# Kernel tuning notes

Measured on AMD Instinct MI355X. Metric: run time of the kernel, lower is better.

The kernel has to match this reference:

```python
import math
import jax
import jax.numpy as jnp
import numpy as np
from jax import lax
from jax.scipy.special import digamma

EPS_RHO = 1e-12
EPS_LOG = 1e-8
BANDWIDTH_FACTOR = 1.06
MIN_BANDWIDTH = 1e-4


def setup_inputs() -> dict:
    key = jax.random.key(0)
    activity = jax.random.uniform(key, (1024, 64), dtype=jnp.float32)  # values in [0,1]
    return {"activity": activity, "k": 5}


def _knn_joint_entropy(activity, k):
    B, N = activity.shape
    # (B, B, N) pairwise differences -> squared distances (B, B)
    diff = activity[:, None, :] - activity[None, :, :]
    dists_sq = jnp.sum(diff * diff, axis=-1)
    # k+1 smallest per row (includes self-distance 0); torch.topk(largest=False) ascending
    neg_topk, _ = lax.top_k(-dists_sq, k + 1)
    rho_sq = jnp.maximum(-neg_topk[:, k], EPS_RHO)
    # log unit-ball volume via lgamma (avoids overflow for large N)
    log_c_d = 0.5 * N * math.log(math.pi) - math.lgamma(N / 2 + 1)
    dg_k = digamma(jnp.float32(k))
    dg_B = digamma(jnp.float32(B))
    log_rho_sum = 0.5 * jnp.mean(jnp.log(rho_sq))
    h_nats = -dg_k + dg_B + log_c_d + N * log_rho_sum
    return h_nats / math.log(2.0)


def _kde_density(samples, query_points, bandwidth_factor):
    B_samples, R = samples.shape
    std = jnp.std(samples, axis=0, ddof=1)  # torch.std uses unbiased (ddof=1)
    h = jnp.maximum(bandwidth_factor * std * B_samples ** (-0.2), MIN_BANDWIDTH)  # (R,)
    X = query_points[:, None, :]  # (B, 1, R)
    Y = samples[None, :, :]       # (1, B, R)
    hr = h[None, None, :]
    norm_factor = math.sqrt(2 * math.pi)
    u_orig = (X - Y) / hr
    u_left = (X + Y) / hr
    u_right = (X - (2.0 - Y)) / hr
    kernel = (jnp.exp(-0.5 * u_orig ** 2)
              + jnp.exp(-0.5 * u_left ** 2)
              + jnp.exp(-0.5 * u_right ** 2)) / norm_factor
    density = jnp.sum(kernel, axis=1) / (B_samples * h[None, :])  # (B, R)
    return density


def _kde_marginal_entropies(activity, bandwidth_factor):
    density = _kde_density(activity, activity, bandwidth_factor)
    log_prob = jnp.log(density + EPS_LOG)
    return -jnp.mean(log_prob, axis=0)  # (R,)


def reference(activity, k):
    joint_h = _knn_joint_entropy(activity, k)            # scalar (bits)
    marginals = _kde_marginal_entropies(activity, BANDWIDTH_FACTOR)  # (N,)
    return jnp.concatenate([joint_h[None], marginals])   # (N+1,)
```

## Files before the change

kernel.cpp:

```cpp
#include <hip/hip_runtime.h>
#include <math.h>

#define BB 1024
#define NN 64

#define LN2F 0.69314718055994530942f
#define TW   128
#define NOUT 514
#define HSIZE 1537

__global__ __launch_bounds__(256, 4) void fused_kernel(const float* __restrict__ act,
                                                       const int* __restrict__ kptr,
                                                       float* __restrict__ logrho,
                                                       float* __restrict__ out) {
    const int bx = blockIdx.x;
    const int tid = threadIdx.x;

    __shared__ float s_d[4096];
    __shared__ float s_x[264];

    if (bx >= 64) {
        const int qbase = (bx - 64) * 4;
        if (tid < 64) {
            ((float4*)s_x)[tid] = ((const float4*)(act + (size_t)qbase * NN))[tid];
        }
        __syncthreads();

        #pragma unroll 1
        for (int c = 0; c < 4; ++c) {
            const int j = tid + 256 * c;
            const float4* row = (const float4*)(act + (size_t)j * NN);
            float a0 = 0.f, a1 = 0.f, a2 = 0.f, a3 = 0.f;
            #pragma unroll 2
            for (int d = 0; d < 16; ++d) {
                const float4 v = row[d];
                {   const float4 qq = ((const float4*)s_x)[d];
                    float x0 = v.x - qq.x, x1 = v.y - qq.y, x2 = v.z - qq.z, x3 = v.w - qq.w;
                    a0 += x0 * x0 + x1 * x1 + x2 * x2 + x3 * x3; }
                {   const float4 qq = ((const float4*)s_x)[16 + d];
                    float x0 = v.x - qq.x, x1 = v.y - qq.y, x2 = v.z - qq.z, x3 = v.w - qq.w;
                    a1 += x0 * x0 + x1 * x1 + x2 * x2 + x3 * x3; }
                {   const float4 qq = ((const float4*)s_x)[32 + d];
                    float x0 = v.x - qq.x, x1 = v.y - qq.y, x2 = v.z - qq.z, x3 = v.w - qq.w;
                    a2 += x0 * x0 + x1 * x1 + x2 * x2 + x3 * x3; }
                {   const float4 qq = ((const float4*)s_x)[48 + d];
                    float x0 = v.x - qq.x, x1 = v.y - qq.y, x2 = v.z - qq.z, x3 = v.w - qq.w;
                    a3 += x0 * x0 + x1 * x1 + x2 * x2 + x3 * x3; }
            }
            s_d[0 * 1024 + j] = a0;
            s_d[1 * 1024 + j] = a1;
            s_d[2 * 1024 + j] = a2;
            s_d[3 * 1024 + j] = a3;
        }
        __syncthreads();

        const int w = tid >> 6, lane = tid & 63;
        float v[16];
        #pragma unroll
        for (int c = 0; c < 16; ++c) v[c] = s_d[w * 1024 + lane + 64 * c];
        const int kk = kptr[0];
        float last = 0.f;
        for (int e = 0; e <= kk; ++e) {
            float bv = 1e30f; int bi = 0;
            #pragma unroll
            for (int c = 0; c < 16; ++c) { if (v[c] < bv) { bv = v[c]; bi = c; } }
            float mv = bv; int mi = (lane << 4) | bi;
            #pragma unroll
            for (int off = 32; off > 0; off >>= 1) {
                float ov = __shfl_xor(mv, off);
                int   oi = __shfl_xor(mi, off);
                if (ov < mv || (ov == mv && oi < mi)) { mv = ov; mi = oi; }
            }
            last = mv;
            if ((mi >> 4) == lane) v[mi & 15] = 1e30f;
        }
        if (lane == 0) {
            logrho[qbase + w] = __builtin_amdgcn_logf(fmaxf(last, 1e-12f)) * LN2F;
        }
    } else {
        const int r = bx;
        float* harr = s_d + 1024;
        int*   hint = (int*)harr;
        float* ktab = s_d + 2564;
        float* outg = s_d + 2696;

        float cv[4];
        float lsum = 0.f, lsq = 0.f;
        #pragma unroll
        for (int c = 0; c < 4; ++c) {
            const int j = tid + 256 * c;
            float v = act[(size_t)j * NN + r];
            cv[c] = v;
            lsum += v; lsq += v * v;
        }
        #pragma unroll
        for (int off = 32; off > 0; off >>= 1) {
            lsum += __shfl_xor(lsum, off);
            lsq  += __shfl_xor(lsq,  off);
        }
        const int wid = tid >> 6;
        if ((tid & 63) == 0) { s_x[wid] = lsum; s_x[4 + wid] = lsq; }

        for (int i = tid; i < HSIZE; i += 256) hint[i] = 0;
        __syncthreads();

        const float total = s_x[0] + s_x[1] + s_x[2] + s_x[3];
        const float totsq = s_x[4] + s_x[5] + s_x[6] + s_x[7];
        const float mean = total * (1.f / BB);
        const float var = (totsq - (float)BB * mean * mean) * (1.f / (BB - 1));
        const float stdv = sqrtf(fmaxf(var, 0.f));
        const float h = fmaxf(1.06f * 0.25f * stdv, 1e-4f);
        const float ih = 1.f / h;
        const float a  = 0.84932180028801904272f * ih;
        const float ad = a * (1.f / 512.f);

        #pragma unroll
        for (int c = 0; c < 4; ++c) {
            const float x = cv[c];
            const int b0 = (int)floorf(x * 512.f) + 512;
            const int b1 = (int)floorf(-x * 512.f) + 512;
            const int b2 = (int)floorf((2.f - x) * 512.f) + 512;
            atomicAdd(&hint[b0], 1);
            atomicAdd(&hint[b1], 1);
            atomicAdd(&hint[b2], 1);
        }
        if (tid <= TW) {
            const float t = ad * (float)tid;
            ktab[tid] = __builtin_amdgcn_exp2f(-(t * t));
        }
        __syncthreads();

        for (int i = tid; i < HSIZE; i += 256) {
            const int c = hint[i];
            harr[i] = (float)c;
        }
        __syncthreads();

        for (int o = tid; o < NOUT; o += 256) {
            const float* hp = harr + 511 + o;
            float acc = hp[0] * ktab[0];
            #pragma unroll 4
            for (int m = 1; m <= TW; ++m)
                acc += (hp[m] + hp[-m]) * ktab[m];
            outg[o] = acc;
        }
        __syncthreads();

        const float dscale = 0.39894228040143267794f * ih * (1.f / (float)BB);
        float lpsum = 0.f;
        #pragma unroll
        for (int c = 0; c < 4; ++c) {
            const float u = fmaf(cv[c], 512.f, 511.5f);
            const float fu = floorf(u);
            const int i0 = (int)fu - 511;
            const float f = u - fu;
            const float dv = outg[i0] + (outg[i0 + 1] - outg[i0]) * f;
            lpsum += __builtin_amdgcn_logf(fmaf(dv, dscale, 1e-8f)) * LN2F;
        }
        #pragma unroll
        for (int off = 32; off > 0; off >>= 1) lpsum += __shfl_xor(lpsum, off);
        if ((tid & 63) == 0) s_x[8 + wid] = lpsum;
        __syncthreads();
        if (tid == 0) {
            const float tot = s_x[8] + s_x[9] + s_x[10] + s_x[11];
            out[1 + r] = -tot * (1.f / (float)BB);
        }
    }
}

__global__ __launch_bounds__(256) void finalize_kernel(const float* __restrict__ logrho,
                                                       const int* __restrict__ kptr,
                                                       double log_c_d, double dg_B,
                                                       float* __restrict__ out) {
    const int tid = threadIdx.x;
    __shared__ double red[256];

    double s = 0.0;
    #pragma unroll
    for (int c = 0; c < 4; ++c) s += (double)logrho[tid + 256 * c];
    red[tid] = s;
    __syncthreads();
    for (int st = 128; st > 0; st >>= 1) { if (tid < st) red[tid] += red[tid + st]; __syncthreads(); }

    if (tid == 0) {
        const int kk = kptr[0];
        double dgk = -0.57721566490153286061;
        for (int t = 1; t < kk; ++t) dgk += 1.0 / (double)t;
        const double log_rho_sum = 0.5 * (red[0] / (double)BB);
        const double h_nats = -dgk + dg_B + log_c_d + (double)NN * log_rho_sum;
        out[0] = (float)(h_nats / 0.69314718055994530942);
    }
}

extern "C" void kernel_launch(void* const* d_in, const int* in_sizes, int n_in,
                              void* d_out, int out_size, void* d_ws, size_t ws_size,
                              hipStream_t stream) {
    const float* act = (const float*)d_in[0];
    const int* kptr = (const int*)d_in[1];
    float* out = (float*)d_out;

    float* logrho = (float*)d_ws;

    const double log_c_d = 0.5 * (double)NN * log(M_PI) - lgamma((double)NN / 2.0 + 1.0);
    const double xB = (double)BB;
    const double dg_B = log(xB) - 1.0 / (2.0 * xB) - 1.0 / (12.0 * xB * xB)
                        + 1.0 / (120.0 * xB * xB * xB * xB);

    fused_kernel<<<320, 256, 0, stream>>>(act, kptr, logrho, out);
    finalize_kernel<<<1, 256, 0, stream>>>(logrho, kptr, log_c_d, dg_B, out);
}
```

Before: 22.54 us.

## Split KDE blocks into four chunks with coarser histogram and partial sums

The KDE branch now runs four blocks per marginal dimension, each evaluating log-density for one quarter of the samples and writing a partial sum that the finalize kernel reduces. The binned histogram resolution is halved (256 bins per unit, kernel half-width 64), which cuts the convolution work per block. KNN blocks move to the front of the grid. The trade-offs are that each chunk block redundantly recomputes the statistics, the histogram and the convolution, and that the coarser binning lowers density accuracy.

Result: no change. 22.58 us (+0.2%).

```diff
diff --git a/kernel.cpp b/kernel.cpp
--- a/kernel.cpp
+++ b/kernel.cpp
@@ -5,22 +5,24 @@
 #define NN 64
 
 #define LN2F 0.69314718055994530942f
-#define TW   128
-#define NOUT 514
-#define HSIZE 1537
+#define BINS 256
+#define TW   64
+#define HSIZE 769
+#define NOUT 258
+#define OBASE 255
 
 __global__ __launch_bounds__(256, 4) void fused_kernel(const float* __restrict__ act,
                                                        const int* __restrict__ kptr,
                                                        float* __restrict__ logrho,
-                                                       float* __restrict__ out) {
+                                                       float* __restrict__ partial) {
     const int bx = blockIdx.x;
     const int tid = threadIdx.x;
 
     __shared__ float s_d[4096];
     __shared__ float s_x[264];
 
-    if (bx >= 64) {
-        const int qbase = (bx - 64) * 4;
+    if (bx < 256) {
+        const int qbase = bx * 4;
         if (tid < 64) {
             ((float4*)s_x)[tid] = ((const float4*)(act + (size_t)qbase * NN))[tid];
         }
@@ -78,11 +80,14 @@
             logrho[qbase + w] = __builtin_amdgcn_logf(fmaxf(last, 1e-12f)) * LN2F;
         }
     } else {
-        const int r = bx;
-        float* harr = s_d + 1024;
-        int*   hint = (int*)harr;
-        float* ktab = s_d + 2564;
-        float* outg = s_d + 2696;
+        const int idx = bx - 256;
+        const int r = idx >> 2;
+        const int chunk = idx & 3;
+
+        int*   hint = (int*)s_d;
+        float* harr = s_d;
+        float* ktab = s_d + 772;
+        float* outg = s_d + 840;
 
         float cv[4];
         float lsum = 0.f, lsq = 0.f;
@@ -112,14 +117,17 @@
         const float h = fmaxf(1.06f * 0.25f * stdv, 1e-4f);
         const float ih = 1.f / h;
         const float a  = 0.84932180028801904272f * ih;
-        const float ad = a * (1.f / 512.f);
+        const float ad = a * (1.f / (float)BINS);
 
         #pragma unroll
         for (int c = 0; c < 4; ++c) {
             const float x = cv[c];
-            const int b0 = (int)floorf(x * 512.f) + 512;
-            const int b1 = (int)floorf(-x * 512.f) + 512;
-            const int b2 = (int)floorf((2.f - x) * 512.f) + 512;
+            int b0 = (int)floorf(x * (float)BINS) + BINS;
+            int b1 = (int)floorf(-x * (float)BINS) + BINS;
+            int b2 = (int)floorf((2.f - x) * (float)BINS) + BINS;
+            b0 = min(max(b0, 0), HSIZE - 1);
+            b1 = min(max(b1, 0), HSIZE - 1);
+            b2 = min(max(b2, 0), HSIZE - 1);
             atomicAdd(&hint[b0], 1);
             atomicAdd(&hint[b1], 1);
             atomicAdd(&hint[b2], 1);
@@ -137,7 +145,7 @@
         __syncthreads();
 
         for (int o = tid; o < NOUT; o += 256) {
-            const float* hp = harr + 511 + o;
+            const float* hp = harr + OBASE + o;
             float acc = hp[0] * ktab[0];
             #pragma unroll 4
             for (int m = 1; m <= TW; ++m)
@@ -147,28 +155,26 @@
         __syncthreads();
 
         const float dscale = 0.39894228040143267794f * ih * (1.f / (float)BB);
-        float lpsum = 0.f;
-        #pragma unroll
-        for (int c = 0; c < 4; ++c) {
-            const float u = fmaf(cv[c], 512.f, 511.5f);
-            const float fu = floorf(u);
-            const int i0 = (int)fu - 511;
-            const float f = u - fu;
-            const float dv = outg[i0] + (outg[i0 + 1] - outg[i0]) * f;
-            lpsum += __builtin_amdgcn_logf(fmaf(dv, dscale, 1e-8f)) * LN2F;
-        }
-        #pragma unroll
-        for (int off = 32; off > 0; off >>= 1) lpsum += __shfl_xor(lpsum, off);
-        if ((tid & 63) == 0) s_x[8 + wid] = lpsum;
+        const float x = cv[chunk];
+        const float u = fmaf(x, (float)BINS, (float)OBASE + 0.5f);
+        const float fu = floorf(u);
+        const int i0 = (int)fu - OBASE;
+        const float f = u - fu;
+        const float dv = outg[i0] + (outg[i0 + 1] - outg[i0]) * f;
+        float lp = __builtin_amdgcn_logf(fmaf(dv, dscale, 1e-8f)) * LN2F;
+
+        #pragma unroll
+        for (int off = 32; off > 0; off >>= 1) lp += __shfl_xor(lp, off);
+        if ((tid & 63) == 0) s_x[8 + wid] = lp;
         __syncthreads();
         if (tid == 0) {
-            const float tot = s_x[8] + s_x[9] + s_x[10] + s_x[11];
-            out[1 + r] = -tot * (1.f / (float)BB);
+            partial[idx] = s_x[8] + s_x[9] + s_x[10] + s_x[11];
         }
     }
 }
 
 __global__ __launch_bounds__(256) void finalize_kernel(const float* __restrict__ logrho,
+                                                       const float* __restrict__ partial,
                                                        const int* __restrict__ kptr,
                                                        double log_c_d, double dg_B,
                                                        float* __restrict__ out) {
@@ -190,6 +196,11 @@
         const double h_nats = -dgk + dg_B + log_c_d + (double)NN * log_rho_sum;
         out[0] = (float)(h_nats / 0.69314718055994530942);
     }
+    if (tid < NN) {
+        const float p = partial[tid * 4 + 0] + partial[tid * 4 + 1]
+                      + partial[tid * 4 + 2] + partial[tid * 4 + 3];
+        out[1 + tid] = -p * (1.0f / (float)BB);
+    }
 }
 
 extern "C" void kernel_launch(void* const* d_in, const int* in_sizes, int n_in,
@@ -200,12 +211,13 @@
     float* out = (float*)d_out;
 
     float* logrho = (float*)d_ws;
+    float* partial = logrho + BB;
 
     const double log_c_d = 0.5 * (double)NN * log(M_PI) - lgamma((double)NN / 2.0 + 1.0);
     const double xB = (double)BB;
     const double dg_B = log(xB) - 1.0 / (2.0 * xB) - 1.0 / (12.0 * xB * xB)
                         + 1.0 / (120.0 * xB * xB * xB * xB);
 
-    fused_kernel<<<320, 256, 0, stream>>>(act, kptr, logrho, out);
-    finalize_kernel<<<1, 256, 0, stream>>>(logrho, kptr, log_c_d, dg_B, out);
+    fused_kernel<<<512, 256, 0, stream>>>(act, kptr, logrho, partial);
+    finalize_kernel<<<1, 256, 0, stream>>>(logrho, partial, kptr, log_c_d, dg_B, out);
 }
```
